# Optimization experiments

Measured on AMD Instinct MI355X. Metric: run time of the kernel, lower is better.

Reference implementation:

```python
import jax, jax.numpy as jnp
import numpy as np

DIM = 384
K = 64               # num_classes
TEMP = 0.1
BASE_TEMP = 2.0
LAMB = 25.0
PIXEL_SIZE = 50      # pixel_update_freq * 5
K_BAN = 10
SINKHORN_ITERS = 3
BS, N = 16, 512


def _l2norm(x, eps=1e-12):
    return x / jnp.maximum(jnp.linalg.norm(x, axis=-1, keepdims=True), eps)


def _online_clustering(scores):
    # SwAV-style Sinkhorn in log space on lamb-scaled cosine logits, then argmax.
    logq = scores
    for _ in range(SINKHORN_ITERS):
        logq = logq - jax.scipy.special.logsumexp(logq, axis=1, keepdims=True)
        logq = logq - jax.scipy.special.logsumexp(logq, axis=0, keepdims=True)
    return jnp.argmax(logq, axis=1)


def _supcon(anchor, y_anchor, contrast, y_contrast, exclude_diag, require_pos):
    # mask[i,j] = 1 if same label
    mask = (y_anchor[:, None] == y_contrast[None, :]).astype(anchor.dtype)
    logits = (anchor @ contrast.T) / TEMP
    logits = logits - jax.lax.stop_gradient(jnp.max(logits, axis=1, keepdims=True))
    if exclude_diag:
        mask = mask * (1.0 - jnp.eye(anchor.shape[0], dtype=anchor.dtype))
    exp_logits = jnp.exp(logits)
    # note: neg_mask = 1 - mask, so for exclude_diag the self term counts as negative (faithful)
    neg = (exp_logits * (1.0 - mask)).sum(axis=1, keepdims=True)
    log_prob = logits - jnp.log(exp_logits + neg)
    pos_cnt = mask.sum(axis=1)
    num = (mask * log_prob).sum(axis=1)
    if require_pos:
        valid = (pos_cnt > 0).astype(anchor.dtype)
        mlpp = jnp.where(pos_cnt > 0, num / jnp.maximum(pos_cnt, 1.0), 0.0)
        return -(TEMP / BASE_TEMP) * jnp.sum(mlpp) / jnp.maximum(valid.sum(), 1.0)
    return jnp.mean(-(TEMP / BASE_TEMP) * num / pos_cnt)


def _forward(feats, off_feats, cluster_center, point_queue):
    bs, n, dim = off_feats.shape
    n_off = _l2norm(off_feats.reshape(-1, dim))
    cluster_feats = jnp.concatenate([n_off, point_queue.reshape(-1, dim)], axis=0)
    log_alpha = cluster_feats @ cluster_center.T              # (bs*n + K*PIXEL_SIZE, K)
    labels = _online_clustering(log_alpha * LAMB)[: bs * n]
    f = _l2norm(feats).reshape(-1, dim)
    # ppc2: anchors vs sampled queue entries (same random column indices for every class)
    k_samp = PIXEL_SIZE - K_BAN
    idx = jax.random.permutation(jax.random.key(1), PIXEL_SIZE)[:k_samp]
    x_c = point_queue[:, idx, :].reshape(-1, dim)             # (K*k_samp, dim)
    y_c = jnp.repeat(jnp.arange(K), k_samp)
    loss = _supcon(f, labels, x_c, y_c, exclude_diag=False, require_pos=False)
    # ppc: anchors vs anchors, diagonal removed from positives
    loss = loss + _supcon(f, labels, f, labels, exclude_diag=True, require_pos=True)
    return loss


def setup_inputs() -> dict:
    key = jax.random.key(0)
    k1, k2, k3, k4 = jax.random.split(key, 4)
    feats = jax.random.normal(k1, (BS, N, DIM), dtype=jnp.float32)
    off_feats = jax.random.normal(k2, (BS, N, DIM), dtype=jnp.float32)
    cluster_center = _l2norm(jax.random.normal(k3, (K, DIM), dtype=jnp.float32))
    point_queue = _l2norm(jax.random.normal(k4, (K, PIXEL_SIZE, DIM), dtype=jnp.float32))
    return {"feats": feats, "off_feats": off_feats,
            "cluster_center": cluster_center, "point_queue": point_queue}


def reference(feats, off_feats, cluster_center, point_queue):
    return _forward(feats, off_feats, cluster_center, point_queue)
```

## Files before the change

kernel.cpp:

```cpp
#include <hip/hip_runtime.h>
#include <stdint.h>
#include <algorithm>

#define DIM   384
#define KCLS  64
#define NPIX  50
#define KSAMP 40
#define NANCH 8192
#define NQ    3200
#define NTOT  11392
#define NXC   2560

typedef __attribute__((ext_vector_type(8)))  short s16x8;
typedef __attribute__((ext_vector_type(16))) float f32x16;

struct Idx40 { int v[KSAMP]; };

__device__ __forceinline__ float wave_sum64(float v){
  #pragma unroll
  for (int o = 32; o >= 1; o >>= 1) v += __shfl_xor(v, o);
  return v;
}

__device__ __forceinline__ unsigned short f2bf(float x){
  union { float f; uint32_t u; } c; c.f = x;
  uint32_t r = c.u + 0x7FFFu + ((c.u >> 16) & 1u);
  if ((c.u & 0x7F800000u) == 0x7F800000u) r = c.u;
  return (unsigned short)(r >> 16);
}

__device__ __forceinline__ float bf2f(unsigned short h){
  union { uint32_t u; float f; } c; c.u = ((uint32_t)h) << 16;
  return c.f;
}

__device__ __forceinline__ void split_hl(float x, unsigned short& hi, unsigned short& lo){
  hi = f2bf(x);
  lo = f2bf(x - bf2f(hi));
}

__device__ __forceinline__ void gload16(const unsigned short* g, unsigned short* l){
  __builtin_amdgcn_global_load_lds(
      (const __attribute__((address_space(1))) unsigned int*)g,
      (__attribute__((address_space(3))) unsigned int*)l, 16, 0, 0);
}

__global__ __launch_bounds__(256) void norm_copy_k(const float* __restrict__ feats,
    const float* __restrict__ off, const float* __restrict__ pq,
    const float* __restrict__ CC,
    unsigned short* __restrict__ fNh,
    unsigned short* __restrict__ CFhi, unsigned short* __restrict__ CFlo,
    unsigned short* __restrict__ cchi, unsigned short* __restrict__ cclo,
    unsigned short* __restrict__ xch, Idx40 idx){
  int row  = blockIdx.x * 4 + (threadIdx.x >> 6);
  int lane = threadIdx.x & 63;
  if (row < 2 * NANCH){
    const float* src = (row < NANCH) ? feats + (size_t)row * DIM
                                     : off + (size_t)(row - NANCH) * DIM;
    float v[6]; float ss = 0.f;
    #pragma unroll
    for (int e = 0; e < 6; e++){ v[e] = src[lane + 64 * e]; ss += v[e] * v[e]; }
    ss = wave_sum64(ss);
    float inv = 1.f / fmaxf(sqrtf(ss), 1e-12f);
    if (row < NANCH){
      unsigned short* dh = fNh + (size_t)row * DIM;
      #pragma unroll
      for (int e = 0; e < 6; e++) dh[lane + 64 * e] = f2bf(v[e] * inv);
    } else {
      size_t base = (size_t)(row - NANCH) * DIM;
      #pragma unroll
      for (int e = 0; e < 6; e++){
        unsigned short h, l;
        split_hl(v[e] * inv, h, l);
        CFhi[base + lane + 64 * e] = h;
        CFlo[base + lane + 64 * e] = l;
      }
    }
  } else if (row < 2 * NANCH + NQ){
    int q = row - 2 * NANCH;
    const float* src = pq + (size_t)q * DIM;
    size_t base = (size_t)(NANCH + q) * DIM;
    #pragma unroll
    for (int e = 0; e < 6; e++){
      unsigned short h, l;
      split_hl(src[lane + 64 * e], h, l);
      CFhi[base + lane + 64 * e] = h;
      CFlo[base + lane + 64 * e] = l;
    }
  } else if (row < 2 * NANCH + NQ + KCLS){
    int r = row - 2 * NANCH - NQ;
    size_t base = (size_t)r * DIM;
    #pragma unroll
    for (int e = 0; e < 6; e++){
      unsigned short h, l;
      split_hl(CC[base + lane + 64 * e], h, l);
      cchi[base + lane + 64 * e] = h;
      cclo[base + lane + 64 * e] = l;
    }
  } else {
    int q = row - 2 * NANCH - NQ - KCLS;
    int c = q / KSAMP, t = q - c * KSAMP;
    const float* src = pq + ((size_t)c * NPIX + idx.v[t]) * DIM;
    unsigned short* dst = xch + (size_t)q * DIM;
    #pragma unroll
    for (int e = 0; e < 6; e++) dst[lane + 64 * e] = f2bf(src[lane + 64 * e]);
  }
}

__global__ __launch_bounds__(256) void gemm_logq_mfma_k(
    const unsigned short* __restrict__ Ahi, const unsigned short* __restrict__ Alo,
    const unsigned short* __restrict__ Bhi, const unsigned short* __restrict__ Blo,
    float* __restrict__ logq){
  __shared__ unsigned short lAh[128 * 64], lAl[128 * 64];
  __shared__ unsigned short lBh[64 * 64],  lBl[64 * 64];
  int t = threadIdx.x;
  int lane = t & 63, w = t >> 6;
  int l31 = lane & 31, half = lane >> 5;
  int i0 = blockIdx.x * 128;

  int rA = w * 32 + l31;
  int swA = ((rA & 7) << 4);
  int rB0 = l31, rB1 = 32 + l31;
  int swB = ((l31 & 7) << 4);

  f32x16 acc0, acc1;
  #pragma unroll
  for (int r = 0; r < 16; r++){ acc0[r] = 0.f; acc1[r] = 0.f; }

  for (int kc = 0; kc < 6; kc++){
    __syncthreads();
    #pragma unroll
    for (int p = 0; p < 4; p++){
      int c = t + p * 256;
      int row = c >> 3, col = c & 7;
      int sw = ((col << 4) ^ ((row & 7) << 4));
      *(s16x8*)((char*)lAh + row * 128 + sw) =
          *(const s16x8*)(Ahi + (size_t)(i0 + row) * DIM + kc * 64 + col * 8);
      *(s16x8*)((char*)lAl + row * 128 + sw) =
          *(const s16x8*)(Alo + (size_t)(i0 + row) * DIM + kc * 64 + col * 8);
    }
    #pragma unroll
    for (int p = 0; p < 2; p++){
      int c = t + p * 256;
      int row = c >> 3, col = c & 7;
      int sw = ((col << 4) ^ ((row & 7) << 4));
      *(s16x8*)((char*)lBh + row * 128 + sw) =
          *(const s16x8*)(Bhi + (size_t)row * DIM + kc * 64 + col * 8);
      *(s16x8*)((char*)lBl + row * 128 + sw) =
          *(const s16x8*)(Blo + (size_t)row * DIM + kc * 64 + col * 8);
    }
    __syncthreads();
    #pragma unroll
    for (int kk = 0; kk < 4; kk++){
      int kb = kk * 32 + half * 16;
      s16x8 fah  = *(const s16x8*)((char*)lAh + rA * 128 + (kb ^ swA));
      s16x8 fal  = *(const s16x8*)((char*)lAl + rA * 128 + (kb ^ swA));
      s16x8 fb0h = *(const s16x8*)((char*)lBh + rB0 * 128 + (kb ^ swB));
      s16x8 fb0l = *(const s16x8*)((char*)lBl + rB0 * 128 + (kb ^ swB));
      s16x8 fb1h = *(const s16x8*)((char*)lBh + rB1 * 128 + (kb ^ swB));
      s16x8 fb1l = *(const s16x8*)((char*)lBl + rB1 * 128 + (kb ^ swB));
      acc0 = __builtin_amdgcn_mfma_f32_32x32x16_bf16(fah, fb0h, acc0, 0, 0, 0);
      acc0 = __builtin_amdgcn_mfma_f32_32x32x16_bf16(fah, fb0l, acc0, 0, 0, 0);
      acc0 = __builtin_amdgcn_mfma_f32_32x32x16_bf16(fal, fb0h, acc0, 0, 0, 0);
      acc1 = __builtin_amdgcn_mfma_f32_32x32x16_bf16(fah, fb1h, acc1, 0, 0, 0);
      acc1 = __builtin_amdgcn_mfma_f32_32x32x16_bf16(fah, fb1l, acc1, 0, 0, 0);
      acc1 = __builtin_amdgcn_mfma_f32_32x32x16_bf16(fal, fb1h, acc1, 0, 0, 0);
    }
  }
  #pragma unroll
  for (int r = 0; r < 16; r++){
    int rowp = (r & 3) + 8 * (r >> 2) + 4 * half;
    size_t row = (size_t)(i0 + w * 32 + rowp);
    logq[row * KCLS + l31]      = 25.f * acc0[r];
    logq[row * KCLS + 32 + l31] = 25.f * acc1[r];
  }
}

__global__ __launch_bounds__(256) void rowpass_k(float* __restrict__ logq,
    const float* __restrict__ colsum, int useCol){
  int row  = blockIdx.x * 4 + (threadIdx.x >> 6);
  int lane = threadIdx.x & 63;
  float v = logq[(size_t)row * KCLS + lane];
  if (useCol) v -= logf(colsum[lane]);
  float m = v;
  #pragma unroll
  for (int o = 32; o >= 1; o >>= 1) m = fmaxf(m, __shfl_xor(m, o));
  float s = expf(v - m);
  s = wave_sum64(s);
  logq[(size_t)row * KCLS + lane] = v - (m + logf(s));
}

__global__ __launch_bounds__(256) void colsum_k(const float* __restrict__ logq,
    float* __restrict__ cs){
  int r0 = blockIdx.x * 128;
  int t = threadIdx.x, lane = t & 63, grp = t >> 6;
  float acc = 0.f;
  for (int r = grp; r < 128; r += 4)
    acc += __expf(logq[(size_t)(r0 + r) * KCLS + lane]);
  __shared__ float red[4][64];
  red[grp][lane] = acc;
  __syncthreads();
  if (t < 64) atomicAdd(&cs[t], red[0][t] + red[1][t] + red[2][t] + red[3][t]);
}

__global__ __launch_bounds__(256) void argmax_k(const float* __restrict__ logq,
    const float* __restrict__ cs, int* __restrict__ labels, int* __restrict__ cnt){
  __shared__ float clog[KCLS];
  int t = threadIdx.x;
  if (t < KCLS) clog[t] = logf(cs[t]);
  __syncthreads();
  int i = blockIdx.x * 256 + t;
  if (i >= NANCH) return;
  float best = -INFINITY; int bj = 0;
  for (int j = 0; j < KCLS; j++){
    float v = logq[(size_t)i * KCLS + j] - clog[j];
    if (v > best){ best = v; bj = j; }
  }
  labels[i] = bj;
  atomicAdd(&cnt[bj], 1);
}

__global__ void scan_k(const int* cnt, int* offs, int* offw){
  if (threadIdx.x == 0){
    int acc = 0;
    for (int c = 0; c < KCLS; c++){ offs[c] = acc; offw[c] = acc; acc += cnt[c]; }
  }
}

__global__ __launch_bounds__(256) void scatter_k(const int* __restrict__ labels,
    int* offw, int* __restrict__ sorted, const float* __restrict__ S,
    const float* __restrict__ S2, float* __restrict__ Sp, float* __restrict__ S2p){
  int i = blockIdx.x * 256 + threadIdx.x;
  if (i >= NANCH) return;
  int p = atomicAdd(&offw[labels[i]], 1);
  sorted[p] = i;
  Sp[p]  = S[i];
  S2p[p] = S2[i];
}

__global__ __launch_bounds__(256) void sortrows_k(const unsigned short* __restrict__ fNh,
    const int* __restrict__ sorted, unsigned short* __restrict__ fNs){
  int p = blockIdx.x * 4 + (threadIdx.x >> 6);
  int lane = threadIdx.x & 63;
  int src = sorted[p];
  const uint32_t* s = (const uint32_t*)(fNh + (size_t)src * DIM);
  uint32_t* d = (uint32_t*)(fNs + (size_t)p * DIM);
  #pragma unroll
  for (int e = 0; e < 3; e++) d[lane + 64 * e] = s[lane + 64 * e];
}

__global__ __launch_bounds__(256) void rowsums2_k(
    const unsigned short* __restrict__ A, const unsigned short* __restrict__ Bxc,
    float* __restrict__ S, float* __restrict__ S2){
  int bi = blockIdx.x, y = blockIdx.y;
  const unsigned short* Bp; float* dst;
  int d0 = 0, bjx0 = 0, njt; bool selfpart;
  if (y < 8){
    selfpart = true; Bp = A; dst = S; d0 = y * 4; njt = 4;
  } else if (y == 8){
    if (bi >= 32) return;
    selfpart = true; Bp = A; dst = S; d0 = 32; njt = 1;
  } else {
    selfpart = false; Bp = Bxc; dst = S2; bjx0 = (y - 9) * 4; njt = 4;
  }

  __shared__ unsigned short lds[2][2][128 * 64];
  int t = threadIdx.x, lane = t & 63, w = t >> 6;
  int wr = w >> 1, wc = w & 1;
  int l31 = lane & 31, half = lane >> 5;
  int i0 = bi * 128;
  int lrow = lane >> 3, srcslot = (lane & 7) ^ lrow;
  size_t loff = (size_t)lrow * DIM + srcslot * 8;

  int rA0 = wr * 64 + l31, rA1 = rA0 + 32;
  int rB0 = wc * 64 + l31, rB1 = rB0 + 32;
  int swA = ((rA0 & 7) << 4), swB = ((rB0 & 7) << 4);

  auto jcol = [&](int jt) -> int {
    if (selfpart){ int js = bi + d0 + jt; return (js & 63) * 128; }
    return (bjx0 + jt) * 128;
  };

  f32x16 s0, s1, a00, a01, a10, a11;
  #pragma unroll
  for (int r = 0; r < 16; r++){ s0[r] = 0.f; s1[r] = 0.f; }

  {
    int j0 = jcol(0);
    #pragma unroll
    for (int c = 0; c < 4; c++){
      int chunk = w * 4 + c;
      gload16(A  + (size_t)(i0 + chunk * 8) * DIM + loff, &lds[0][0][chunk * 512]);
      gload16(Bp + (size_t)(j0 + chunk * 8) * DIM + loff, &lds[0][1][chunk * 512]);
    }
  }
  __syncthreads();

  int total = njt * 6;
  int buf = 0;
  for (int s = 0; s < total; s++){
    int jt = s / 6, kc = s - jt * 6;
    if (s + 1 < total){
      int sn = s + 1;
      int jt1 = sn / 6, kc1 = sn - jt1 * 6;
      int j1 = jcol(jt1);
      int nb = buf ^ 1;
      #pragma unroll
      for (int c = 0; c < 4; c++){
        int chunk = w * 4 + c;
        gload16(A  + (size_t)(i0 + chunk * 8) * DIM + kc1 * 64 + loff, &lds[nb][0][chunk * 512]);
        gload16(Bp + (size_t)(j1 + chunk * 8) * DIM + kc1 * 64 + loff, &lds[nb][1][chunk * 512]);
      }
    }
    if (kc == 0){
      #pragma unroll
      for (int r = 0; r < 16; r++){ a00[r] = 0.f; a01[r] = 0.f; a10[r] = 0.f; a11[r] = 0.f; }
    }
    const char* bA = (const char*)&lds[buf][0][0];
    const char* bB = (const char*)&lds[buf][1][0];
    #pragma unroll
    for (int kk = 0; kk < 4; kk++){
      int kb = kk * 32 + half * 16;
      s16x8 fa0 = *(const s16x8*)(bA + rA0 * 128 + (kb ^ swA));
      s16x8 fa1 = *(const s16x8*)(bA + rA1 * 128 + (kb ^ swA));
      s16x8 fb0 = *(const s16x8*)(bB + rB0 * 128 + (kb ^ swB));
      s16x8 fb1 = *(const s16x8*)(bB + rB1 * 128 + (kb ^ swB));
      a00 = __builtin_amdgcn_mfma_f32_32x32x16_bf16(fa0, fb0, a00, 0, 0, 0);
      a01 = __builtin_amdgcn_mfma_f32_32x32x16_bf16(fa0, fb1, a01, 0, 0, 0);
      a10 = __builtin_amdgcn_mfma_f32_32x32x16_bf16(fa1, fb0, a10, 0, 0, 0);
      a11 = __builtin_amdgcn_mfma_f32_32x32x16_bf16(fa1, fb1, a11, 0, 0, 0);
    }
    if (kc == 5){
      int j0 = jcol(jt);
      bool docol = selfpart && (d0 + jt != 0);
      float c0 = 0.f, c1 = 0.f;
      #pragma unroll
      for (int r = 0; r < 16; r++){
        float e00 = __expf(fmaf(a00[r], 10.f, -10.f));
        float e01 = __expf(fmaf(a01[r], 10.f, -10.f));
        float e10 = __expf(fmaf(a10[r], 10.f, -10.f));
        float e11 = __expf(fmaf(a11[r], 10.f, -10.f));
        s0[r] += e00 + e01;
        s1[r] += e10 + e11;
        c0 += e00 + e10;
        c1 += e01 + e11;
      }
      if (docol){
        c0 += __shfl_xor(c0, 32);
        c1 += __shfl_xor(c1, 32);
        if (half == 0){
          atomicAdd(&dst[j0 + wc * 64 + l31], c0);
          atomicAdd(&dst[j0 + wc * 64 + 32 + l31], c1);
        }
      }
    }
    __syncthreads();
    buf ^= 1;
  }

  #pragma unroll
  for (int o = 1; o < 32; o <<= 1){
    #pragma unroll
    for (int r = 0; r < 16; r++){
      s0[r] += __shfl_xor(s0[r], o);
      s1[r] += __shfl_xor(s1[r], o);
    }
  }
  if (l31 == 0){
    #pragma unroll
    for (int r = 0; r < 16; r++){
      int rowp = (r & 3) + 8 * (r >> 2) + 4 * half;
      atomicAdd(&dst[i0 + wr * 64 + rowp], s0[r]);
      atomicAdd(&dst[i0 + wr * 64 + 32 + rowp], s1[r]);
    }
  }
}

__device__ __forceinline__ void gram2(const s16x8* afr,
    const unsigned short* b0, const unsigned short* b1, f32x16& acc0, f32x16& acc1){
  #pragma unroll
  for (int ks = 0; ks < 24; ks++){
    s16x8 v0 = *(const s16x8*)(b0 + ks * 16);
    s16x8 v1 = *(const s16x8*)(b1 + ks * 16);
    acc0 = __builtin_amdgcn_mfma_f32_32x32x16_bf16(afr[ks], v0, acc0, 0, 0, 0);
    acc1 = __builtin_amdgcn_mfma_f32_32x32x16_bf16(afr[ks], v1, acc1, 0, 0, 0);
  }
}

__global__ __launch_bounds__(64) void classpair_k(
    const unsigned short* __restrict__ fNs, const unsigned short* __restrict__ xch,
    const int* __restrict__ offs, const int* __restrict__ cnt,
    const float* __restrict__ S, const float* __restrict__ S2,
    float* __restrict__ num2A, float* __restrict__ mlppA, float* __restrict__ validA){
  int c = blockIdx.x;
  int n = cnt[c], o0 = offs[c];
  if (n == 0) return;
  int lane = threadIdx.x;
  int l31 = lane & 31, half = lane >> 5;
  int ntiles = (n + 31) >> 5;

  for (int rt = blockIdx.y; rt < ntiles; rt += gridDim.y){
    int rpos = rt * 32 + l31;
    const unsigned short* arow = fNs + (size_t)(o0 + (rpos < n ? rpos : 0)) * DIM + half * 8;
    s16x8 afr[24];
    #pragma unroll
    for (int ks = 0; ks < 24; ks++) afr[ks] = *(const s16x8*)(arow + ks * 16);

    f32x16 p20, p21;
    #pragma unroll
    for (int r = 0; r < 16; r++){ p20[r] = 0.f; p21[r] = 0.f; }
    {
      int c1 = 32 + l31;
      const unsigned short* b0 = xch + ((size_t)c * KSAMP + l31) * DIM + half * 8;
      const unsigned short* b1 = xch + ((size_t)c * KSAMP + (c1 < KSAMP ? c1 : 0)) * DIM + half * 8;
      gram2(afr, b0, b1, p20, p21);
    }
    f32x16 red;
    #pragma unroll
    for (int r = 0; r < 16; r++){
      float v0 = expf(fmaf(p20[r], 10.f, -10.f));
      float v1 = (l31 < 8) ? expf(fmaf(p21[r], 10.f, -10.f)) : 0.f;
      red[r] = v0 + v1;
    }
    #pragma unroll
    for (int o = 1; o < 32; o <<= 1)
      #pragma unroll
      for (int r = 0; r < 16; r++) red[r] += __shfl_xor(red[r], o);
    float neg2[16];
    #pragma unroll
    for (int r = 0; r < 16; r++){
      int rowp = (r & 3) + 8 * (r >> 2) + 4 * half;
      int rp = rt * 32 + rowp;
      neg2[r] = (rp < n) ? S2[o0 + rp] - red[r] : 1.f;
    }
    #pragma unroll
    for (int r = 0; r < 16; r++){
      float l0 = fmaf(p20[r], 10.f, -10.f);
      float l1 = fmaf(p21[r], 10.f, -10.f);
      float a = l0 - logf(expf(l0) + neg2[r]);
      float b = (l31 < 8) ? l1 - logf(expf(l1) + neg2[r]) : 0.f;
      red[r] = a + b;
    }
    #pragma unroll
    for (int o = 1; o < 32; o <<= 1)
      #pragma unroll
      for (int r = 0; r < 16; r++) red[r] += __shfl_xor(red[r], o);
    if (l31 == 0){
      #pragma unroll
      for (int r = 0; r < 16; r++){
        int rowp = (r & 3) + 8 * (r >> 2) + 4 * half;
        int rp = rt * 32 + rowp;
        if (rp < n) num2A[o0 + rp] = red[r];
      }
    }

    f32x16 pe;
    #pragma unroll
    for (int r = 0; r < 16; r++) pe[r] = 0.f;
    for (int ct = 0; ct < ntiles; ct += 2){
      int cp0 = ct * 32 + l31;
      int cp1 = (ct + 1) * 32 + l31;
      bool has1 = (ct + 1) < ntiles;
      const unsigned short* b0 = fNs + (size_t)(o0 + (cp0 < n ? cp0 : 0)) * DIM + half * 8;
      const unsigned short* b1 = fNs + (size_t)(o0 + (has1 && cp1 < n ? cp1 : 0)) * DIM + half * 8;
      f32x16 a0, a1;
      #pragma unroll
      for (int r = 0; r < 16; r++){ a0[r] = 0.f; a1[r] = 0.f; }
      gram2(afr, b0, b1, a0, a1);
      #pragma unroll
      for (int r = 0; r < 16; r++){
        int rowp = (r & 3) + 8 * (r >> 2) + 4 * half;
        int rp = rt * 32 + rowp;
        if (cp0 < n && cp0 != rp) pe[r] += expf(fmaf(a0[r], 10.f, -10.f));
        if (has1 && cp1 < n && cp1 != rp) pe[r] += expf(fmaf(a1[r], 10.f, -10.f));
      }
    }
    #pragma unroll
    for (int o = 1; o < 32; o <<= 1)
      #pragma unroll
      for (int r = 0; r < 16; r++) pe[r] += __shfl_xor(pe[r], o);
    float neg[16];
    #pragma unroll
    for (int r = 0; r < 16; r++){
      int rowp = (r & 3) + 8 * (r >> 2) + 4 * half;
      int rp = rt * 32 + rowp;
      neg[r] = (rp < n) ? S[o0 + rp] - pe[r] : 1.f;
    }

    f32x16 nm;
    #pragma unroll
    for (int r = 0; r < 16; r++) nm[r] = 0.f;
    for (int ct = 0; ct < ntiles; ct += 2){
      int cp0 = ct * 32 + l31;
      int cp1 = (ct + 1) * 32 + l31;
      bool has1 = (ct + 1) < ntiles;
      const unsigned short* b0 = fNs + (size_t)(o0 + (cp0 < n ? cp0 : 0)) * DIM + half * 8;
      const unsigned short* b1 = fNs + (size_t)(o0 + (has1 && cp1 < n ? cp1 : 0)) * DIM + half * 8;
      f32x16 a0, a1;
      #pragma unroll
      for (int r = 0; r < 16; r++){ a0[r] = 0.f; a1[r] = 0.f; }
      gram2(afr, b0, b1, a0, a1);
      #pragma unroll
      for (int r = 0; r < 16; r++){
        int rowp = (r & 3) + 8 * (r >> 2) + 4 * half;
        int rp = rt * 32 + rowp;
        if (cp0 < n && cp0 != rp){
          float l = fmaf(a0[r], 10.f, -10.f);
          nm[r] += l - logf(expf(l) + neg[r]);
        }
        if (has1 && cp1 < n && cp1 != rp){
          float l = fmaf(a1[r], 10.f, -10.f);
          nm[r] += l - logf(expf(l) + neg[r]);
        }
      }
    }
    #pragma unroll
    for (int o = 1; o < 32; o <<= 1)
      #pragma unroll
      for (int r = 0; r < 16; r++) nm[r] += __shfl_xor(nm[r], o);
    if (l31 == 0){
      #pragma unroll
      for (int r = 0; r < 16; r++){
        int rowp = (r & 3) + 8 * (r >> 2) + 4 * half;
        int rp = rt * 32 + rowp;
        if (rp < n){
          if (n > 1){ mlppA[o0 + rp] = nm[r] / (float)(n - 1); validA[o0 + rp] = 1.f; }
          else      { mlppA[o0 + rp] = 0.f; validA[o0 + rp] = 0.f; }
        }
      }
    }
  }
}

__global__ __launch_bounds__(256) void finalize_k(const float* __restrict__ num2A,
    const float* __restrict__ mlppA, const float* __restrict__ validA,
    float* __restrict__ out){
  int t = threadIdx.x;
  float s2 = 0.f, sm = 0.f, sv = 0.f;
  for (int i = t; i < NANCH; i += 256){ s2 += num2A[i]; sm += mlppA[i]; sv += validA[i]; }
  __shared__ float a2[256], am[256], av[256];
  a2[t] = s2; am[t] = sm; av[t] = sv; __syncthreads();
  for (int o = 128; o >= 1; o >>= 1){
    if (t < o){ a2[t] += a2[t+o]; am[t] += am[t+o]; av[t] += av[t+o]; }
    __syncthreads();
  }
  if (t == 0){
    float loss1 = -0.05f * a2[0] / (40.f * (float)NANCH);
    float loss2 = -0.05f * am[0] / fmaxf(av[0], 1.f);
    out[0] = loss1 + loss2;
  }
}

static void tf2x32(uint32_t k0, uint32_t k1, uint32_t x0, uint32_t x1, uint32_t out[2]){
  uint32_t ks[3] = { k0, k1, k0 ^ k1 ^ 0x1BD11BDAu };
  static const int R[2][4] = { {13,15,26,6}, {17,29,16,24} };
  x0 += ks[0]; x1 += ks[1];
  for (int i = 0; i < 5; i++){
    for (int j = 0; j < 4; j++){
      x0 += x1;
      int r = R[i & 1][j];
      x1 = (x1 << r) | (x1 >> (32 - r));
      x1 ^= x0;
    }
    x0 += ks[(i + 1) % 3];
    x1 += ks[(i + 2) % 3] + (uint32_t)(i + 1);
  }
  out[0] = x0; out[1] = x1;
}

static void compute_idx(int idx_out[KSAMP]){
  uint32_t p0[2], p1[2];
  tf2x32(0u, 1u, 0u, 2u, p0);
  tf2x32(0u, 1u, 1u, 3u, p1);
  uint32_t sk0 = p0[1], sk1 = p1[1];
  uint32_t bits[NPIX];
  for (int i = 0; i < 25; i++){
    uint32_t o[2];
    tf2x32(sk0, sk1, (uint32_t)i, (uint32_t)(25 + i), o);
    bits[i] = o[0]; bits[25 + i] = o[1];
  }
  int perm[NPIX];
  for (int i = 0; i < NPIX; i++) perm[i] = i;
  std::stable_sort(perm, perm + NPIX, [&](int a, int b){ return bits[a] < bits[b]; });
  for (int i = 0; i < KSAMP; i++) idx_out[i] = perm[i];
}

extern "C" void kernel_launch(void* const* d_in, const int* in_sizes, int n_in,
                              void* d_out, int out_size, void* d_ws, size_t ws_size,
                              hipStream_t stream){
  const float* feats = (const float*)d_in[0];
  const float* off   = (const float*)d_in[1];
  const float* cc    = (const float*)d_in[2];
  const float* pq    = (const float*)d_in[3];
  float* out = (float*)d_out;

  char* ws = (char*)d_ws;
  size_t ofs = 0;
  auto alloc = [&](size_t bytes) -> void* {
    ofs = (ofs + 255) & ~(size_t)255;
    void* p = ws + ofs;
    ofs += bytes;
    return p;
  };
  float* logq   = (float*)alloc((size_t)NTOT * KCLS * 4);
  unsigned short* fNh  = (unsigned short*)alloc((size_t)NANCH * DIM * 2);
  unsigned short* fNs  = (unsigned short*)alloc((size_t)NANCH * DIM * 2);
  unsigned short* CFhi = (unsigned short*)alloc((size_t)NTOT * DIM * 2);
  unsigned short* CFlo = (unsigned short*)alloc((size_t)NTOT * DIM * 2);
  unsigned short* cchi = (unsigned short*)alloc((size_t)KCLS * DIM * 2);
  unsigned short* cclo = (unsigned short*)alloc((size_t)KCLS * DIM * 2);
  unsigned short* xch  = (unsigned short*)alloc((size_t)NXC * DIM * 2);
  float* S2     = (float*)alloc((2 * NANCH + KCLS + 3 * KCLS) * 4);
  float* S      = S2 + NANCH;
  int*   cnt    = (int*)(S2 + 2 * NANCH);
  float* cs0    = S2 + 2 * NANCH + KCLS;
  float* cs1    = cs0 + KCLS;
  float* cs2    = cs1 + KCLS;
  float* Sp     = (float*)alloc(NANCH * 4);
  float* S2p    = (float*)alloc(NANCH * 4);
  float* num2A  = (float*)alloc(NANCH * 4);
  float* mlppA  = (float*)alloc(NANCH * 4);
  float* validA = (float*)alloc(NANCH * 4);
  int* labels   = (int*)alloc(NANCH * 4);
  int* sorted   = (int*)alloc(NANCH * 4);
  int* offs     = (int*)alloc(KCLS * 4);
  int* offw     = (int*)alloc(KCLS * 4);

  Idx40 idx;
  compute_idx(idx.v);

  hipMemsetAsync(S2, 0, (2 * NANCH + 4 * KCLS) * 4, stream);
  norm_copy_k<<<(2 * NANCH + NQ + KCLS + NXC) / 4, 256, 0, stream>>>(
      feats, off, pq, cc, fNh, CFhi, CFlo, cchi, cclo, xch, idx);
  rowsums2_k<<<dim3(64, 14), 256, 0, stream>>>(fNh, xch, S, S2);
  gemm_logq_mfma_k<<<NTOT / 128, 256, 0, stream>>>(CFhi, CFlo, cchi, cclo, logq);
  rowpass_k<<<NTOT / 4, 256, 0, stream>>>(logq, cs0, 0);
  colsum_k<<<NTOT / 128, 256, 0, stream>>>(logq, cs0);
  rowpass_k<<<NTOT / 4, 256, 0, stream>>>(logq, cs0, 1);
  colsum_k<<<NTOT / 128, 256, 0, stream>>>(logq, cs1);
  rowpass_k<<<NTOT / 4, 256, 0, stream>>>(logq, cs1, 1);
  colsum_k<<<NTOT / 128, 256, 0, stream>>>(logq, cs2);
  argmax_k<<<NANCH / 256, 256, 0, stream>>>(logq, cs2, labels, cnt);
  scan_k<<<1, 64, 0, stream>>>(cnt, offs, offw);
  scatter_k<<<NANCH / 256, 256, 0, stream>>>(labels, offw, sorted, S, S2, Sp, S2p);
  sortrows_k<<<NANCH / 4, 256, 0, stream>>>(fNh, sorted, fNs);
  classpair_k<<<dim3(KCLS, 8), 64, 0, stream>>>(fNs, xch, offs, cnt, Sp, S2p,
                                                num2A, mlppA, validA);
  finalize_k<<<1, 256, 0, stream>>>(num2A, mlppA, validA, out);
}
```

Measured before the change: 239.0 us.

## Fuse Sinkhorn row and column passes into GEMM epilogue and combined kernels

```diff
diff --git a/kernel.cpp b/kernel.cpp
--- a/kernel.cpp
+++ b/kernel.cpp
@@ -55,64 +55,81 @@
   int row  = blockIdx.x * 4 + (threadIdx.x >> 6);
   int lane = threadIdx.x & 63;
   if (row < 2 * NANCH){
-    const float* src = (row < NANCH) ? feats + (size_t)row * DIM
-                                     : off + (size_t)(row - NANCH) * DIM;
-    float v[6]; float ss = 0.f;
-    #pragma unroll
-    for (int e = 0; e < 6; e++){ v[e] = src[lane + 64 * e]; ss += v[e] * v[e]; }
+    const float2* src = (const float2*)((row < NANCH) ? feats + (size_t)row * DIM
+                                                      : off + (size_t)(row - NANCH) * DIM);
+    float2 v[3]; float ss = 0.f;
+    #pragma unroll
+    for (int e = 0; e < 3; e++){
+      v[e] = src[lane + 64 * e];
+      ss += v[e].x * v[e].x + v[e].y * v[e].y;
+    }
     ss = wave_sum64(ss);
     float inv = 1.f / fmaxf(sqrtf(ss), 1e-12f);
     if (row < NANCH){
-      unsigned short* dh = fNh + (size_t)row * DIM;
-      #pragma unroll
-      for (int e = 0; e < 6; e++) dh[lane + 64 * e] = f2bf(v[e] * inv);
+      uint32_t* dh = (uint32_t*)(fNh + (size_t)row * DIM);
+      #pragma unroll
+      for (int e = 0; e < 3; e++)
+        dh[lane + 64 * e] = (uint32_t)f2bf(v[e].x * inv) | ((uint32_t)f2bf(v[e].y * inv) << 16);
     } else {
-      size_t base = (size_t)(row - NANCH) * DIM;
-      #pragma unroll
-      for (int e = 0; e < 6; e++){
-        unsigned short h, l;
-        split_hl(v[e] * inv, h, l);
-        CFhi[base + lane + 64 * e] = h;
-        CFlo[base + lane + 64 * e] = l;
+      uint32_t* dhh = (uint32_t*)(CFhi + (size_t)(row - NANCH) * DIM);
+      uint32_t* dhl = (uint32_t*)(CFlo + (size_t)(row - NANCH) * DIM);
+      #pragma unroll
+      for (int e = 0; e < 3; e++){
+        unsigned short hx, lx, hy, ly;
+        split_hl(v[e].x * inv, hx, lx);
+        split_hl(v[e].y * inv, hy, ly);
+        dhh[lane + 64 * e] = (uint32_t)hx | ((uint32_t)hy << 16);
+        dhl[lane + 64 * e] = (uint32_t)lx | ((uint32_t)ly << 16);
       }
     }
   } else if (row < 2 * NANCH + NQ){
     int q = row - 2 * NANCH;
-    const float* src = pq + (size_t)q * DIM;
-    size_t base = (size_t)(NANCH + q) * DIM;
-    #pragma unroll
-    for (int e = 0; e < 6; e++){
-      unsigned short h, l;
-      split_hl(src[lane + 64 * e], h, l);
-      CFhi[base + lane + 64 * e] = h;
-      CFlo[base + lane + 64 * e] = l;
+    const float2* src = (const float2*)(pq + (size_t)q * DIM);
+    uint32_t* dhh = (uint32_t*)(CFhi + (size_t)(NANCH + q) * DIM);
+    uint32_t* dhl = (uint32_t*)(CFlo + (size_t)(NANCH + q) * DIM);
+    #pragma unroll
+    for (int e = 0; e < 3; e++){
+      float2 v = src[lane + 64 * e];
+      unsigned short hx, lx, hy, ly;
+      split_hl(v.x, hx, lx);
+      split_hl(v.y, hy, ly);
+      dhh[lane + 64 * e] = (uint32_t)hx | ((uint32_t)hy << 16);
+      dhl[lane + 64 * e] = (uint32_t)lx | ((uint32_t)ly << 16);
     }
   } else if (row < 2 * NANCH + NQ + KCLS){
     int r = row - 2 * NANCH - NQ;
-    size_t base = (size_t)r * DIM;
-    #pragma unroll
-    for (int e = 0; e < 6; e++){
-      unsigned short h, l;
-      split_hl(CC[base + lane + 64 * e], h, l);
-      cchi[base + lane + 64 * e] = h;
-      cclo[base + lane + 64 * e] = l;
+    const float2* src = (const float2*)(CC + (size_t)r * DIM);
+    uint32_t* dhh = (uint32_t*)(cchi + (size_t)r * DIM);
+    uint32_t* dhl = (uint32_t*)(cclo + (size_t)r * DIM);
+    #pragma unroll
+    for (int e = 0; e < 3; e++){
+      float2 v = src[lane + 64 * e];
+      unsigned short hx, lx, hy, ly;
+      split_hl(v.x, hx, lx);
+      split_hl(v.y, hy, ly);
+      dhh[lane + 64 * e] = (uint32_t)hx | ((uint32_t)hy << 16);
+      dhl[lane + 64 * e] = (uint32_t)lx | ((uint32_t)ly << 16);
     }
   } else {
     int q = row - 2 * NANCH - NQ - KCLS;
     int c = q / KSAMP, t = q - c * KSAMP;
-    const float* src = pq + ((size_t)c * NPIX + idx.v[t]) * DIM;
-    unsigned short* dst = xch + (size_t)q * DIM;
-    #pragma unroll
-    for (int e = 0; e < 6; e++) dst[lane + 64 * e] = f2bf(src[lane + 64 * e]);
+    const float2* src = (const float2*)(pq + ((size_t)c * NPIX + idx.v[t]) * DIM);
+    uint32_t* dst = (uint32_t*)(xch + (size_t)q * DIM);
+    #pragma unroll
+    for (int e = 0; e < 3; e++){
+      float2 v = src[lane + 64 * e];
+      dst[lane + 64 * e] = (uint32_t)f2bf(v.x) | ((uint32_t)f2bf(v.y) << 16);
+    }
   }
 }
 
 __global__ __launch_bounds__(256) void gemm_logq_mfma_k(
     const unsigned short* __restrict__ Ahi, const unsigned short* __restrict__ Alo,
     const unsigned short* __restrict__ Bhi, const unsigned short* __restrict__ Blo,
-    float* __restrict__ logq){
+    float* __restrict__ logq, float* __restrict__ cs0){
   __shared__ unsigned short lAh[128 * 64], lAl[128 * 64];
   __shared__ unsigned short lBh[64 * 64],  lBl[64 * 64];
+  __shared__ float red[4][64];
   int t = threadIdx.x;
   int lane = t & 63, w = t >> 6;
   int l31 = lane & 31, half = lane >> 5;
@@ -167,40 +184,57 @@
       acc1 = __builtin_amdgcn_mfma_f32_32x32x16_bf16(fal, fb1h, acc1, 0, 0, 0);
     }
   }
+
+  float colacc0 = 0.f, colacc1 = 0.f;
   #pragma unroll
   for (int r = 0; r < 16; r++){
+    float v0 = 25.f * acc0[r];
+    float v1 = 25.f * acc1[r];
+    float m = fmaxf(v0, v1);
+    #pragma unroll
+    for (int o = 16; o >= 1; o >>= 1) m = fmaxf(m, __shfl_xor(m, o));
+    float e0 = expf(v0 - m), e1 = expf(v1 - m);
+    float s = e0 + e1;
+    #pragma unroll
+    for (int o = 16; o >= 1; o >>= 1) s += __shfl_xor(s, o);
+    float ls = m + logf(s);
     int rowp = (r & 3) + 8 * (r >> 2) + 4 * half;
     size_t row = (size_t)(i0 + w * 32 + rowp);
-    logq[row * KCLS + l31]      = 25.f * acc0[r];
-    logq[row * KCLS + 32 + l31] = 25.f * acc1[r];
-  }
-}
-
-__global__ __launch_bounds__(256) void rowpass_k(float* __restrict__ logq,
-    const float* __restrict__ colsum, int useCol){
-  int row  = blockIdx.x * 4 + (threadIdx.x >> 6);
-  int lane = threadIdx.x & 63;
-  float v = logq[(size_t)row * KCLS + lane];
-  if (useCol) v -= logf(colsum[lane]);
-  float m = v;
-  #pragma unroll
-  for (int o = 32; o >= 1; o >>= 1) m = fmaxf(m, __shfl_xor(m, o));
-  float s = expf(v - m);
-  s = wave_sum64(s);
-  logq[(size_t)row * KCLS + lane] = v - (m + logf(s));
-}
-
-__global__ __launch_bounds__(256) void colsum_k(const float* __restrict__ logq,
-    float* __restrict__ cs){
-  int r0 = blockIdx.x * 128;
-  int t = threadIdx.x, lane = t & 63, grp = t >> 6;
-  float acc = 0.f;
-  for (int r = grp; r < 128; r += 4)
-    acc += __expf(logq[(size_t)(r0 + r) * KCLS + lane]);
+    logq[row * KCLS + l31]      = v0 - ls;
+    logq[row * KCLS + 32 + l31] = v1 - ls;
+    float inv = 1.f / s;
+    colacc0 += e0 * inv;
+    colacc1 += e1 * inv;
+  }
+  colacc0 += __shfl_xor(colacc0, 32);
+  colacc1 += __shfl_xor(colacc1, 32);
+  if (half == 0){ red[w][l31] = colacc0; red[w][32 + l31] = colacc1; }
+  __syncthreads();
+  if (t < 64) atomicAdd(&cs0[t], red[0][t] + red[1][t] + red[2][t] + red[3][t]);
+}
+
+__global__ __launch_bounds__(256) void rowcol_k(float* __restrict__ logq,
+    const float* __restrict__ csPrev, float* __restrict__ csNext){
+  int r0 = blockIdx.x * 16;
+  int t = threadIdx.x, lane = t & 63, w = t >> 6;
+  float cl = logf(csPrev[lane]);
+  float colacc = 0.f;
+  #pragma unroll
+  for (int r = w; r < 16; r += 4){
+    size_t off = (size_t)(r0 + r) * KCLS + lane;
+    float v = logq[off] - cl;
+    float m = v;
+    #pragma unroll
+    for (int o = 32; o >= 1; o >>= 1) m = fmaxf(m, __shfl_xor(m, o));
+    float e = expf(v - m);
+    float s = wave_sum64(e);
+    logq[off] = v - (m + logf(s));
+    colacc += e / s;
+  }
   __shared__ float red[4][64];
-  red[grp][lane] = acc;
+  red[w][lane] = colacc;
   __syncthreads();
-  if (t < 64) atomicAdd(&cs[t], red[0][t] + red[1][t] + red[2][t] + red[3][t]);
+  if (t < 64) atomicAdd(&csNext[t], red[0][t] + red[1][t] + red[2][t] + red[3][t]);
 }
 
 __global__ __launch_bounds__(256) void argmax_k(const float* __restrict__ logq,
@@ -633,13 +667,9 @@
   norm_copy_k<<<(2 * NANCH + NQ + KCLS + NXC) / 4, 256, 0, stream>>>(
       feats, off, pq, cc, fNh, CFhi, CFlo, cchi, cclo, xch, idx);
   rowsums2_k<<<dim3(64, 14), 256, 0, stream>>>(fNh, xch, S, S2);
-  gemm_logq_mfma_k<<<NTOT / 128, 256, 0, stream>>>(CFhi, CFlo, cchi, cclo, logq);
-  rowpass_k<<<NTOT / 4, 256, 0, stream>>>(logq, cs0, 0);
-  colsum_k<<<NTOT / 128, 256, 0, stream>>>(logq, cs0);
-  rowpass_k<<<NTOT / 4, 256, 0, stream>>>(logq, cs0, 1);
-  colsum_k<<<NTOT / 128, 256, 0, stream>>>(logq, cs1);
-  rowpass_k<<<NTOT / 4, 256, 0, stream>>>(logq, cs1, 1);
-  colsum_k<<<NTOT / 128, 256, 0, stream>>>(logq, cs2);
+  gemm_logq_mfma_k<<<NTOT / 128, 256, 0, stream>>>(CFhi, CFlo, cchi, cclo, logq, cs0);
+  rowcol_k<<<NTOT / 16, 256, 0, stream>>>(logq, cs0, cs1);
+  rowcol_k<<<NTOT / 16, 256, 0, stream>>>(logq, cs1, cs2);
   argmax_k<<<NANCH / 256, 256, 0, stream>>>(logq, cs2, labels, cnt);
   scan_k<<<1, 64, 0, stream>>>(cnt, offs, offw);
   scatter_k<<<NANCH / 256, 256, 0, stream>>>(labels, offw, sorted, S, S2, Sp, S2p);
```

After: 262.3 us. 9.7% more time.

## Restructure rowsums GEMM to reuse A fragments across two column tiles

Applied to the files above, without the earlier changes.

```diff
diff --git a/kernel.cpp b/kernel.cpp
--- a/kernel.cpp
+++ b/kernel.cpp
@@ -255,16 +255,17 @@
   int bi = blockIdx.x, y = blockIdx.y;
   const unsigned short* Bp; float* dst;
   int d0 = 0, bjx0 = 0, njt; bool selfpart;
-  if (y < 8){
-    selfpart = true; Bp = A; dst = S; d0 = y * 4; njt = 4;
-  } else if (y == 8){
+  if (y < 16){
+    selfpart = true; Bp = A; dst = S; d0 = y * 2; njt = 2;
+  } else if (y == 16){
     if (bi >= 32) return;
     selfpart = true; Bp = A; dst = S; d0 = 32; njt = 1;
   } else {
-    selfpart = false; Bp = Bxc; dst = S2; bjx0 = (y - 9) * 4; njt = 4;
-  }
-
-  __shared__ unsigned short lds[2][2][128 * 64];
+    selfpart = false; Bp = Bxc; dst = S2; bjx0 = (y - 17) * 2; njt = 2;
+  }
+
+  __shared__ unsigned short lA[2][128 * 64];
+  __shared__ unsigned short lB[2][128 * 64];
   int t = threadIdx.x, lane = t & 63, w = t >> 6;
   int wr = w >> 1, wc = w & 1;
   int l31 = lane & 31, half = lane >> 5;
@@ -276,86 +277,134 @@
   int rB0 = wc * 64 + l31, rB1 = rB0 + 32;
   int swA = ((rA0 & 7) << 4), swB = ((rB0 & 7) << 4);
 
-  auto jcol = [&](int jt) -> int {
-    if (selfpart){ int js = bi + d0 + jt; return (js & 63) * 128; }
-    return (bjx0 + jt) * 128;
-  };
-
-  f32x16 s0, s1, a00, a01, a10, a11;
-  #pragma unroll
-  for (int r = 0; r < 16; r++){ s0[r] = 0.f; s1[r] = 0.f; }
-
-  {
-    int j0 = jcol(0);
+  int jc0 = selfpart ? ((bi + d0) & 63) * 128     : bjx0 * 128;
+  int jc1 = selfpart ? ((bi + d0 + 1) & 63) * 128 : (bjx0 + 1) * 128;
+
+  auto stageA = [&](int kc, int ab){
     #pragma unroll
     for (int c = 0; c < 4; c++){
       int chunk = w * 4 + c;
-      gload16(A  + (size_t)(i0 + chunk * 8) * DIM + loff, &lds[0][0][chunk * 512]);
-      gload16(Bp + (size_t)(j0 + chunk * 8) * DIM + loff, &lds[0][1][chunk * 512]);
-    }
-  }
-  __syncthreads();
-
-  int total = njt * 6;
-  int buf = 0;
-  for (int s = 0; s < total; s++){
-    int jt = s / 6, kc = s - jt * 6;
-    if (s + 1 < total){
-      int sn = s + 1;
-      int jt1 = sn / 6, kc1 = sn - jt1 * 6;
-      int j1 = jcol(jt1);
-      int nb = buf ^ 1;
-      #pragma unroll
-      for (int c = 0; c < 4; c++){
-        int chunk = w * 4 + c;
-        gload16(A  + (size_t)(i0 + chunk * 8) * DIM + kc1 * 64 + loff, &lds[nb][0][chunk * 512]);
-        gload16(Bp + (size_t)(j1 + chunk * 8) * DIM + kc1 * 64 + loff, &lds[nb][1][chunk * 512]);
-      }
-    }
-    if (kc == 0){
-      #pragma unroll
-      for (int r = 0; r < 16; r++){ a00[r] = 0.f; a01[r] = 0.f; a10[r] = 0.f; a11[r] = 0.f; }
-    }
-    const char* bA = (const char*)&lds[buf][0][0];
-    const char* bB = (const char*)&lds[buf][1][0];
+      gload16(A + (size_t)(i0 + chunk * 8) * DIM + kc * 64 + loff, &lA[ab][chunk * 512]);
+    }
+  };
+  auto stageB = [&](int j0, int kc, int sb){
+    #pragma unroll
+    for (int c = 0; c < 4; c++){
+      int chunk = w * 4 + c;
+      gload16(Bp + (size_t)(j0 + chunk * 8) * DIM + kc * 64 + loff, &lB[sb][chunk * 512]);
+    }
+  };
+
+  s16x8 afr0[4], afr1[4];
+  auto loadA = [&](const unsigned short* bA){
     #pragma unroll
     for (int kk = 0; kk < 4; kk++){
       int kb = kk * 32 + half * 16;
-      s16x8 fa0 = *(const s16x8*)(bA + rA0 * 128 + (kb ^ swA));
-      s16x8 fa1 = *(const s16x8*)(bA + rA1 * 128 + (kb ^ swA));
-      s16x8 fb0 = *(const s16x8*)(bB + rB0 * 128 + (kb ^ swB));
-      s16x8 fb1 = *(const s16x8*)(bB + rB1 * 128 + (kb ^ swB));
-      a00 = __builtin_amdgcn_mfma_f32_32x32x16_bf16(fa0, fb0, a00, 0, 0, 0);
-      a01 = __builtin_amdgcn_mfma_f32_32x32x16_bf16(fa0, fb1, a01, 0, 0, 0);
-      a10 = __builtin_amdgcn_mfma_f32_32x32x16_bf16(fa1, fb0, a10, 0, 0, 0);
-      a11 = __builtin_amdgcn_mfma_f32_32x32x16_bf16(fa1, fb1, a11, 0, 0, 0);
-    }
-    if (kc == 5){
-      int j0 = jcol(jt);
-      bool docol = selfpart && (d0 + jt != 0);
-      float c0 = 0.f, c1 = 0.f;
-      #pragma unroll
-      for (int r = 0; r < 16; r++){
-        float e00 = __expf(fmaf(a00[r], 10.f, -10.f));
-        float e01 = __expf(fmaf(a01[r], 10.f, -10.f));
-        float e10 = __expf(fmaf(a10[r], 10.f, -10.f));
-        float e11 = __expf(fmaf(a11[r], 10.f, -10.f));
-        s0[r] += e00 + e01;
-        s1[r] += e10 + e11;
-        c0 += e00 + e10;
-        c1 += e01 + e11;
-      }
-      if (docol){
-        c0 += __shfl_xor(c0, 32);
-        c1 += __shfl_xor(c1, 32);
-        if (half == 0){
-          atomicAdd(&dst[j0 + wc * 64 + l31], c0);
-          atomicAdd(&dst[j0 + wc * 64 + 32 + l31], c1);
-        }
-      }
-    }
+      afr0[kk] = *(const s16x8*)((const char*)bA + rA0 * 128 + (kb ^ swA));
+      afr1[kk] = *(const s16x8*)((const char*)bA + rA1 * 128 + (kb ^ swA));
+    }
+  };
+
+  f32x16 acc0[4], acc1[4];
+  #pragma unroll
+  for (int q = 0; q < 4; q++){
+    #pragma unroll
+    for (int r = 0; r < 16; r++){ acc0[q][r] = 0.f; acc1[q][r] = 0.f; }
+  }
+
+  auto compute = [&](f32x16 (&acc)[4], const unsigned short* bS){
+    #pragma unroll
+    for (int kk = 0; kk < 4; kk++){
+      int kb = kk * 32 + half * 16;
+      s16x8 fb0 = *(const s16x8*)((const char*)bS + rB0 * 128 + (kb ^ swB));
+      s16x8 fb1 = *(const s16x8*)((const char*)bS + rB1 * 128 + (kb ^ swB));
+      acc[0] = __builtin_amdgcn_mfma_f32_32x32x16_bf16(afr0[kk], fb0, acc[0], 0, 0, 0);
+      acc[1] = __builtin_amdgcn_mfma_f32_32x32x16_bf16(afr0[kk], fb1, acc[1], 0, 0, 0);
+      acc[2] = __builtin_amdgcn_mfma_f32_32x32x16_bf16(afr1[kk], fb0, acc[2], 0, 0, 0);
+      acc[3] = __builtin_amdgcn_mfma_f32_32x32x16_bf16(afr1[kk], fb1, acc[3], 0, 0, 0);
+    }
+  };
+
+  if (njt == 2){
+    stageA(0, 0);
+    stageB(jc0, 0, 0);
+    stageB(jc1, 0, 1);
     __syncthreads();
-    buf ^= 1;
+    for (int kc = 0; kc < 6; kc++){
+      if (kc >= 1) stageB(jc1, kc, 1);
+      loadA(lA[kc & 1]);
+      compute(acc0, lB[0]);
+      __syncthreads();
+      if (kc <= 4){
+        stageB(jc0, kc + 1, 0);
+        stageA(kc + 1, (kc + 1) & 1);
+      }
+      compute(acc1, lB[1]);
+      __syncthreads();
+    }
+  } else {
+    stageA(0, 0);
+    stageB(jc0, 0, 0);
+    __syncthreads();
+    for (int kc = 0; kc < 6; kc++){
+      if (kc <= 4){
+        stageB(jc0, kc + 1, (kc + 1) & 1);
+        stageA(kc + 1, (kc + 1) & 1);
+      }
+      loadA(lA[kc & 1]);
+      compute(acc0, lB[kc & 1]);
+      __syncthreads();
+    }
+  }
+
+  f32x16 s0, s1;
+  #pragma unroll
+  for (int r = 0; r < 16; r++){ s0[r] = 0.f; s1[r] = 0.f; }
+  {
+    bool docol = selfpart && (d0 != 0);
+    float c0 = 0.f, c1 = 0.f;
+    #pragma unroll
+    for (int r = 0; r < 16; r++){
+      float e00 = __expf(fmaf(acc0[0][r], 10.f, -10.f));
+      float e01 = __expf(fmaf(acc0[1][r], 10.f, -10.f));
+      float e10 = __expf(fmaf(acc0[2][r], 10.f, -10.f));
+      float e11 = __expf(fmaf(acc0[3][r], 10.f, -10.f));
+      s0[r] += e00 + e01;
+      s1[r] += e10 + e11;
+      c0 += e00 + e10;
+      c1 += e01 + e11;
+    }
+    if (docol){
+      c0 += __shfl_xor(c0, 32);
+      c1 += __shfl_xor(c1, 32);
+      if (half == 0){
+        atomicAdd(&dst[jc0 + wc * 64 + l31], c0);
+        atomicAdd(&dst[jc0 + wc * 64 + 32 + l31], c1);
+      }
+    }
+  }
+  if (njt == 2){
+    bool docol = selfpart;
+    float c0 = 0.f, c1 = 0.f;
+    #pragma unroll
+    for (int r = 0; r < 16; r++){
+      float e00 = __expf(fmaf(acc1[0][r], 10.f, -10.f));
+      float e01 = __expf(fmaf(acc1[1][r], 10.f, -10.f));
+      float e10 = __expf(fmaf(acc1[2][r], 10.f, -10.f));
+      float e11 = __expf(fmaf(acc1[3][r], 10.f, -10.f));
+      s0[r] += e00 + e01;
+      s1[r] += e10 + e11;
+      c0 += e00 + e10;
+      c1 += e01 + e11;
+    }
+    if (docol){
+      c0 += __shfl_xor(c0, 32);
+      c1 += __shfl_xor(c1, 32);
+      if (half == 0){
+        atomicAdd(&dst[jc1 + wc * 64 + l31], c0);
+        atomicAdd(&dst[jc1 + wc * 64 + 32 + l31], c1);
+      }
+    }
   }
 
   #pragma unroll
@@ -632,7 +681,7 @@
   hipMemsetAsync(S2, 0, (2 * NANCH + 4 * KCLS) * 4, stream);
   norm_copy_k<<<(2 * NANCH + NQ + KCLS + NXC) / 4, 256, 0, stream>>>(
       feats, off, pq, cc, fNh, CFhi, CFlo, cchi, cclo, xch, idx);
-  rowsums2_k<<<dim3(64, 14), 256, 0, stream>>>(fNh, xch, S, S2);
+  rowsums2_k<<<dim3(64, 27), 256, 0, stream>>>(fNh, xch, S, S2);
   gemm_logq_mfma_k<<<NTOT / 128, 256, 0, stream>>>(CFhi, CFlo, cchi, cclo, logq);
   rowpass_k<<<NTOT / 4, 256, 0, stream>>>(logq, cs0, 0);
   colsum_k<<<NTOT / 128, 256, 0, stream>>>(logq, cs0);
```

Result: slower. 266.8 us (+11.6%).
